# Kernel optimization log

Measured on AMD Instinct MI355X. Metric: run time of the kernel, lower is better.

Reference implementation:

```python
import jax, jax.numpy as jnp
import numpy as np

DIM = 512
NUM_HEADS = 8
HEAD_DIM = DIM // NUM_HEADS


def setup_inputs() -> dict:
    key = jax.random.key(0)
    ks = jax.random.split(key, 9)
    s = 1.0 / np.sqrt(DIM)
    x = jax.random.normal(ks[0], (2, 4096, DIM), dtype=jnp.float32)
    Wq = jax.random.uniform(ks[1], (DIM, DIM), jnp.float32, -s, s)
    bq = jax.random.uniform(ks[2], (DIM,), jnp.float32, -s, s)
    Wk = jax.random.uniform(ks[3], (DIM, DIM), jnp.float32, -s, s)
    bk = jax.random.uniform(ks[4], (DIM,), jnp.float32, -s, s)
    Wv = jax.random.uniform(ks[5], (DIM, DIM), jnp.float32, -s, s)
    bv = jax.random.uniform(ks[6], (DIM,), jnp.float32, -s, s)
    Wo = jax.random.uniform(ks[7], (DIM, DIM), jnp.float32, -s, s)
    bo = jax.random.uniform(ks[8], (DIM,), jnp.float32, -s, s)
    return {"x": x, "Wq": Wq, "bq": bq, "Wk": Wk, "bk": bk,
            "Wv": Wv, "bv": bv, "Wo": Wo, "bo": bo}


def reference(x, Wq, bq, Wk, bk, Wv, bv, Wo, bo):
    B, S, D = x.shape
    H, Hd = NUM_HEADS, HEAD_DIM
    # Linear layers (torch stores weight as [out,in]; here W is [in,out])
    q = (x @ Wq + bq).reshape(B, S, H, Hd).transpose(0, 2, 1, 3)  # [B,H,S,Hd]
    k = (x @ Wk + bk).reshape(B, S, H, Hd).transpose(0, 2, 1, 3)
    v = (x @ Wv + bv).reshape(B, S, H, Hd).transpose(0, 2, 1, 3)
    # NOTE: original scales by dim**0.5, not head_dim**0.5
    energy = jnp.einsum('bhqd,bhkd->bhqk', q, k) / jnp.sqrt(jnp.float32(D))
    attn = jax.nn.softmax(energy, axis=-1)
    out = jnp.einsum('bhqk,bhkd->bhqd', attn, v)
    out = out.transpose(0, 2, 1, 3).reshape(B, S, D)
    return out @ Wo + bo
```

## Files before the change

### kernel.cpp

```cpp
#include <hip/hip_runtime.h>

typedef unsigned short USH;
typedef short s16x8 __attribute__((ext_vector_type(8)));
typedef float f32x4 __attribute__((ext_vector_type(4)));
typedef float f32x4v __attribute__((ext_vector_type(4)));
typedef unsigned int u32x4 __attribute__((ext_vector_type(4)));
typedef s16x8 s16x8_a __attribute__((may_alias));
typedef f32x4v f32x4v_a __attribute__((may_alias));
typedef u32x4 u32x4_a __attribute__((may_alias));
typedef unsigned int u32_a __attribute__((may_alias));
typedef unsigned long long u64_a __attribute__((may_alias));

#if __has_builtin(__builtin_amdgcn_exp2f)
#define EXP2F(x) __builtin_amdgcn_exp2f(x)
#else
#define EXP2F(x) __builtin_exp2f(x)
#endif

__device__ __forceinline__ USH f2bf(float f) {
  union { float f; unsigned int i; } c; c.f = f;
  unsigned int x = c.i;
  return (USH)((x + 0x7FFFu + ((x >> 16) & 1u)) >> 16);
}
__device__ __forceinline__ unsigned int pk_bf16(float a, float b) {
  union { float f; unsigned int i; } ca, cb; ca.f = a; cb.f = b;
  return ((ca.i + 0x8000u) >> 16) | ((cb.i + 0x8000u) & 0xFFFF0000u);
}

__device__ __forceinline__ f32x4 mfma16(s16x8 a, s16x8 b, f32x4 c) {
  return __builtin_amdgcn_mfma_f32_16x16x32_bf16(a, b, c, 0, 0, 0);
}

__global__ void transpose_w(const float* __restrict__ Wq, const float* __restrict__ Wk,
                            const float* __restrict__ Wv, const float* __restrict__ Wo,
                            USH* __restrict__ wsT) {
  __shared__ float tile[32][33];
  const int z = blockIdx.z;
  const float* W = (z == 0) ? Wq : (z == 1) ? Wk : (z == 2) ? Wv : Wo;
  USH* WT = wsT + (size_t)z * 262144;
  const int n0 = blockIdx.x * 32, k0 = blockIdx.y * 32;
  const int tx = threadIdx.x, ty = threadIdx.y;
  #pragma unroll
  for (int i = 0; i < 4; ++i)
    tile[ty + i * 8][tx] = W[(size_t)(k0 + ty + i * 8) * 512 + n0 + tx];
  __syncthreads();
  #pragma unroll
  for (int i = 0; i < 4; ++i)
    WT[(size_t)(n0 + ty + i * 8) * 512 + k0 + tx] = f2bf(tile[tx][ty + i * 8]);
}

__global__ __launch_bounds__(256) void cvt_x(const float* __restrict__ x,
                                             USH* __restrict__ xb) {
  const size_t i = ((size_t)blockIdx.x * 256 + threadIdx.x) * 8;
  const f32x4v a = *(const f32x4v_a*)(x + i);
  const f32x4v b = *(const f32x4v_a*)(x + i + 4);
  u32x4 s;
  s.x = pk_bf16(a.x, a.y); s.y = pk_bf16(a.z, a.w);
  s.z = pk_bf16(b.x, b.y); s.w = pk_bf16(b.z, b.w);
  *(u32x4_a*)(xb + i) = s;
}

template <int MODE>
__global__ __launch_bounds__(256, 2) void gemm_bias(
    const USH* __restrict__ A, const USH* __restrict__ BT0,
    const float* __restrict__ b0, const float* __restrict__ b1,
    const float* __restrict__ b2,
    USH* __restrict__ oQ, USH* __restrict__ oKV, float* __restrict__ oF) {
  __shared__ __align__(16) USH As[128 * 36];
  __shared__ __align__(16) USH Bs[128 * 36];
  const int z = blockIdx.z;
  const USH* BT = BT0 + (size_t)z * 262144;
  const float* bias = (z == 0) ? b0 : ((z == 1) ? b1 : b2);
  USH* outb = (z == 0) ? oQ : (oKV + (size_t)(z - 1) * 4194304);
  const float qs = (MODE == 1 && z == 0) ? 0.06375871528132839f : 1.0f;

  const int t = threadIdx.x;
  const int w = t >> 6, lane = t & 63;
  const int c = lane & 15, g = lane >> 4;
  const int wm = w & 1, wn = w >> 1;
  const int m0 = blockIdx.x * 128, n0 = blockIdx.y * 128;
  const int srow = t >> 1, scol = (t & 1) * 16;

  f32x4 acc[4][4] = {};

  for (int kt = 0; kt < 16; ++kt) {
    __syncthreads();
    {
      const USH* Ap = A + (size_t)(m0 + srow) * 512 + kt * 32 + scol;
      const s16x8 a0 = *(const s16x8_a*)(Ap);
      const s16x8 a1 = *(const s16x8_a*)(Ap + 8);
      *(s16x8_a*)(As + srow * 36 + scol) = a0;
      *(s16x8_a*)(As + srow * 36 + scol + 8) = a1;
      const USH* Bp = BT + (size_t)(n0 + srow) * 512 + kt * 32 + scol;
      const s16x8 bb0 = *(const s16x8_a*)(Bp);
      const s16x8 bb1 = *(const s16x8_a*)(Bp + 8);
      *(s16x8_a*)(Bs + srow * 36 + scol) = bb0;
      *(s16x8_a*)(Bs + srow * 36 + scol + 8) = bb1;
    }
    __syncthreads();
    s16x8 af[4], bfr[4];
    #pragma unroll
    for (int i = 0; i < 4; ++i) {
      af[i]  = *(const s16x8_a*)(As + (wm * 64 + i * 16 + c) * 36 + g * 8);
      bfr[i] = *(const s16x8_a*)(Bs + (wn * 64 + i * 16 + c) * 36 + g * 8);
    }
    #pragma unroll
    for (int mf = 0; mf < 4; ++mf)
      #pragma unroll
      for (int nf = 0; nf < 4; ++nf)
        acc[mf][nf] = mfma16(af[mf], bfr[nf], acc[mf][nf]);
  }

  #pragma unroll
  for (int nf = 0; nf < 4; ++nf) {
    const int n = n0 + wn * 64 + nf * 16 + c;
    const float bv = bias[n];
    #pragma unroll
    for (int mf = 0; mf < 4; ++mf)
      #pragma unroll
      for (int r = 0; r < 4; ++r) {
        const int m = m0 + wm * 64 + mf * 16 + g * 4 + r;
        const float v = (acc[mf][nf][r] + bv) * qs;
        if (MODE == 0) {
          oF[(size_t)m * 512 + n] = v;
        } else {
          const int bb = m >> 12, s = m & 4095, h = n >> 6, hd = n & 63;
          outb[(((size_t)(bb * 8 + h)) * 4096 + s) * 64 + hd] = f2bf(v);
        }
      }
  }
}

__global__ __launch_bounds__(256, 2) void attn(const USH* __restrict__ Qbuf,
                                               const USH* __restrict__ kv,
                                               USH* __restrict__ att) {
  __shared__ __align__(16) USH Ks[2 * 64 * 36];
  __shared__ __align__(16) USH Vt[64 * 76];
  __shared__ __align__(16) USH Ps[4][32 * 76];
  __shared__ float lbuf[4][32];

  const int t = threadIdx.x;
  const int w = t >> 6, lane = t & 63;
  const int c = lane & 15, g = lane >> 4;
  const int bh = blockIdx.y;
  const int bb = bh >> 3, hh = bh & 7;
  const size_t base = (size_t)bh * 262144;
  const USH* Q = Qbuf + base;
  const USH* K = kv + base;
  const USH* V = kv + 4194304 + base;
  const int q0 = blockIdx.x * 128 + w * 32;

  s16x8 qf[2][2];
  #pragma unroll
  for (int colf = 0; colf < 2; ++colf)
    #pragma unroll
    for (int kh = 0; kh < 2; ++kh)
      qf[colf][kh] = *(const s16x8_a*)(Q + (size_t)(q0 + colf * 16 + c) * 64 + kh * 32 + g * 8);

  s16x8 onesf;
  {
    const short one = (short)0x3F80, val = (c == 0) ? one : (short)0;
    #pragma unroll
    for (int j = 0; j < 8; ++j) onesf[j] = val;
  }

  f32x4 o[2][4] = {};
  f32x4 o_l[2] = {};
  const int kr = t >> 2, kc = (t & 3) * 16;

  for (int kt = 0; kt < 64; ++kt) {
    __syncthreads();
    {
      const s16x8 k0 = *(const s16x8_a*)(K + (size_t)(kt * 64 + kr) * 64 + kc);
      const s16x8 k1 = *(const s16x8_a*)(K + (size_t)(kt * 64 + kr) * 64 + kc + 8);
      const int half = kc >> 5, off = kc & 31;
      *(s16x8_a*)(Ks + half * 2304 + kr * 36 + off) = k0;
      *(s16x8_a*)(Ks + half * 2304 + kr * 36 + off + 8) = k1;
    }
    {
      const int rA = 2 * (t & 31), c0v = (t >> 5) * 8;
      const s16x8 v0 = *(const s16x8_a*)(V + (size_t)(kt * 64 + rA) * 64 + c0v);
      const s16x8 v1 = *(const s16x8_a*)(V + (size_t)(kt * 64 + rA + 1) * 64 + c0v);
      #pragma unroll
      for (int j = 0; j < 8; ++j) {
        const unsigned int pk =
            (unsigned int)(USH)v0[j] | (((unsigned int)(USH)v1[j]) << 16);
        *(u32_a*)(&Vt[(c0v + j) * 76 + rA]) = pk;
      }
    }
    __syncthreads();

    f32x4 st[4][2] = {};
    #pragma unroll
    for (int kh = 0; kh < 2; ++kh) {
      s16x8 ak[4];
      #pragma unroll
      for (int kff = 0; kff < 4; ++kff)
        ak[kff] = *(const s16x8_a*)(Ks + kh * 2304 + (kff * 16 + c) * 36 + g * 8);
      #pragma unroll
      for (int kff = 0; kff < 4; ++kff)
        #pragma unroll
        for (int colf = 0; colf < 2; ++colf)
          st[kff][colf] = mfma16(ak[kff], qf[colf][kh], st[kff][colf]);
    }

    #pragma unroll
    for (int colf = 0; colf < 2; ++colf)
      #pragma unroll
      for (int kff = 0; kff < 4; ++kff)
        #pragma unroll
        for (int r = 0; r < 4; ++r)
          st[kff][colf][r] = EXP2F(st[kff][colf][r]);

    #pragma unroll
    for (int colf = 0; colf < 2; ++colf)
      #pragma unroll
      for (int kff = 0; kff < 4; ++kff) {
        const unsigned int lo = pk_bf16(st[kff][colf][0], st[kff][colf][1]);
        const unsigned int hi = pk_bf16(st[kff][colf][2], st[kff][colf][3]);
        const unsigned long long pk64 =
            (unsigned long long)lo | ((unsigned long long)hi << 32);
        *(u64_a*)(&Ps[w][(c + 16 * colf) * 76 + kff * 16 + g * 4]) = pk64;
      }

    #pragma unroll
    for (int kf = 0; kf < 2; ++kf) {
      s16x8 ap[2], bv[4];
      #pragma unroll
      for (int mf = 0; mf < 2; ++mf)
        ap[mf] = *(const s16x8_a*)(&Ps[w][(mf * 16 + c) * 76 + kf * 32 + g * 8]);
      #pragma unroll
      for (int hf = 0; hf < 4; ++hf)
        bv[hf] = *(const s16x8_a*)(&Vt[(c + 16 * hf) * 76 + kf * 32 + g * 8]);
      #pragma unroll
      for (int mf = 0; mf < 2; ++mf) {
        #pragma unroll
        for (int hf = 0; hf < 4; ++hf)
          o[mf][hf] = mfma16(ap[mf], bv[hf], o[mf][hf]);
        o_l[mf] = mfma16(ap[mf], onesf, o_l[mf]);
      }
    }
  }

  if (c == 0) {
    #pragma unroll
    for (int mf = 0; mf < 2; ++mf)
      #pragma unroll
      for (int r = 0; r < 4; ++r)
        lbuf[w][mf * 16 + g * 4 + r] = o_l[mf][r];
  }
  __syncthreads();

  #pragma unroll
  for (int mf = 0; mf < 2; ++mf)
    #pragma unroll
    for (int r = 0; r < 4; ++r) {
      const int ml = mf * 16 + g * 4 + r;
      const float linv = 1.0f / lbuf[w][ml];
      const int qrow = q0 + ml;
      #pragma unroll
      for (int hf = 0; hf < 4; ++hf) {
        const int hd = c + 16 * hf;
        att[((size_t)(bb * 4096 + qrow)) * 512 + hh * 64 + hd] =
            f2bf(o[mf][hf][r] * linv);
      }
    }
}

extern "C" void kernel_launch(void* const* d_in, const int* in_sizes, int n_in,
                              void* d_out, int out_size, void* d_ws, size_t ws_size,
                              hipStream_t stream) {
  (void)in_sizes; (void)n_in; (void)out_size; (void)ws_size;
  const float* x  = (const float*)d_in[0];
  const float* Wq = (const float*)d_in[1];
  const float* bq = (const float*)d_in[2];
  const float* Wk = (const float*)d_in[3];
  const float* bk = (const float*)d_in[4];
  const float* Wv = (const float*)d_in[5];
  const float* bv = (const float*)d_in[6];
  const float* Wo = (const float*)d_in[7];
  const float* bo = (const float*)d_in[8];
  USH* ws  = (USH*)d_ws;
  USH* wT  = ws;
  USH* kv  = ws + 1048576;
  USH* att = ws + 1048576 + 8388608;
  float* outF = (float*)d_out;
  USH* qscratch = (USH*)d_out;
  USH* xb = (USH*)d_out + 4194304;

  transpose_w<<<dim3(16, 16, 4), dim3(32, 8), 0, stream>>>(Wq, Wk, Wv, Wo, wT);
  cvt_x<<<2048, 256, 0, stream>>>(x, xb);
  gemm_bias<1><<<dim3(64, 4, 3), 256, 0, stream>>>(xb, wT, bq, bk, bv,
                                                   qscratch, kv, nullptr);
  attn<<<dim3(32, 16), 256, 0, stream>>>(qscratch, kv, att);
  gemm_bias<0><<<dim3(64, 4, 1), 256, 0, stream>>>(att, wT + 3 * 262144, bo, bo, bo,
                                                   nullptr, nullptr, outF);
}
```

Measured before the change: 232.9 us.

## Prefetch next tiles into registers and store V pre-transposed from projection

The GEMM and attention loops now load the next K-tile's global data into registers before the current tile's compute, so global latency overlaps the MFMA work. The QKV projection writes V in a transposed [bh][hd][s] layout. This lets the attention kernel copy V straight into shared memory with vector stores instead of the per-element transpose-and-pack loop. The cost is extra registers, which may lower occupancy, and strided scalar stores in the V projection epilogue.

```diff
diff --git a/kernel.cpp b/kernel.cpp
--- a/kernel.cpp
+++ b/kernel.cpp
@@ -8,7 +8,6 @@
 typedef s16x8 s16x8_a __attribute__((may_alias));
 typedef f32x4v f32x4v_a __attribute__((may_alias));
 typedef u32x4 u32x4_a __attribute__((may_alias));
-typedef unsigned int u32_a __attribute__((may_alias));
 typedef unsigned long long u64_a __attribute__((may_alias));
 
 #if __has_builtin(__builtin_amdgcn_exp2f)
@@ -83,20 +82,24 @@
 
   f32x4 acc[4][4] = {};
 
+  const USH* Ap0 = A + (size_t)(m0 + srow) * 512 + scol;
+  const USH* Bp0 = BT + (size_t)(n0 + srow) * 512 + scol;
+  s16x8 pa0 = *(const s16x8_a*)(Ap0);
+  s16x8 pa1 = *(const s16x8_a*)(Ap0 + 8);
+  s16x8 pb0 = *(const s16x8_a*)(Bp0);
+  s16x8 pb1 = *(const s16x8_a*)(Bp0 + 8);
+
   for (int kt = 0; kt < 16; ++kt) {
     __syncthreads();
-    {
-      const USH* Ap = A + (size_t)(m0 + srow) * 512 + kt * 32 + scol;
-      const s16x8 a0 = *(const s16x8_a*)(Ap);
-      const s16x8 a1 = *(const s16x8_a*)(Ap + 8);
-      *(s16x8_a*)(As + srow * 36 + scol) = a0;
-      *(s16x8_a*)(As + srow * 36 + scol + 8) = a1;
-      const USH* Bp = BT + (size_t)(n0 + srow) * 512 + kt * 32 + scol;
-      const s16x8 bb0 = *(const s16x8_a*)(Bp);
-      const s16x8 bb1 = *(const s16x8_a*)(Bp + 8);
-      *(s16x8_a*)(Bs + srow * 36 + scol) = bb0;
-      *(s16x8_a*)(Bs + srow * 36 + scol + 8) = bb1;
-    }
+    *(s16x8_a*)(As + srow * 36 + scol) = pa0;
+    *(s16x8_a*)(As + srow * 36 + scol + 8) = pa1;
+    *(s16x8_a*)(Bs + srow * 36 + scol) = pb0;
+    *(s16x8_a*)(Bs + srow * 36 + scol + 8) = pb1;
+    const int ktn = (kt < 15) ? kt + 1 : kt;
+    pa0 = *(const s16x8_a*)(Ap0 + ktn * 32);
+    pa1 = *(const s16x8_a*)(Ap0 + ktn * 32 + 8);
+    pb0 = *(const s16x8_a*)(Bp0 + ktn * 32);
+    pb1 = *(const s16x8_a*)(Bp0 + ktn * 32 + 8);
     __syncthreads();
     s16x8 af[4], bfr[4];
     #pragma unroll
@@ -125,7 +128,10 @@
           oF[(size_t)m * 512 + n] = v;
         } else {
           const int bb = m >> 12, s = m & 4095, h = n >> 6, hd = n & 63;
-          outb[(((size_t)(bb * 8 + h)) * 4096 + s) * 64 + hd] = f2bf(v);
+          if (z == 2)
+            outb[(((size_t)(bb * 8 + h)) * 64 + hd) * 4096 + s] = f2bf(v);
+          else
+            outb[(((size_t)(bb * 8 + h)) * 4096 + s) * 64 + hd] = f2bf(v);
         }
       }
   }
@@ -167,27 +173,26 @@
   f32x4 o[2][4] = {};
   f32x4 o_l[2] = {};
   const int kr = t >> 2, kc = (t & 3) * 16;
+  const USH* Kp0 = K + (size_t)kr * 64 + kc;
+  const USH* Vp0 = V + (size_t)kr * 4096 + kc;
+  const int khalf = kc >> 5, koff = kc & 31;
+
+  s16x8 pk0 = *(const s16x8_a*)(Kp0);
+  s16x8 pk1 = *(const s16x8_a*)(Kp0 + 8);
+  s16x8 pv0 = *(const s16x8_a*)(Vp0);
+  s16x8 pv1 = *(const s16x8_a*)(Vp0 + 8);
 
   for (int kt = 0; kt < 64; ++kt) {
     __syncthreads();
-    {
-      const s16x8 k0 = *(const s16x8_a*)(K + (size_t)(kt * 64 + kr) * 64 + kc);
-      const s16x8 k1 = *(const s16x8_a*)(K + (size_t)(kt * 64 + kr) * 64 + kc + 8);
-      const int half = kc >> 5, off = kc & 31;
-      *(s16x8_a*)(Ks + half * 2304 + kr * 36 + off) = k0;
-      *(s16x8_a*)(Ks + half * 2304 + kr * 36 + off + 8) = k1;
-    }
-    {
-      const int rA = 2 * (t & 31), c0v = (t >> 5) * 8;
-      const s16x8 v0 = *(const s16x8_a*)(V + (size_t)(kt * 64 + rA) * 64 + c0v);
-      const s16x8 v1 = *(const s16x8_a*)(V + (size_t)(kt * 64 + rA + 1) * 64 + c0v);
-      #pragma unroll
-      for (int j = 0; j < 8; ++j) {
-        const unsigned int pk =
-            (unsigned int)(USH)v0[j] | (((unsigned int)(USH)v1[j]) << 16);
-        *(u32_a*)(&Vt[(c0v + j) * 76 + rA]) = pk;
-      }
-    }
+    *(s16x8_a*)(Ks + khalf * 2304 + kr * 36 + koff) = pk0;
+    *(s16x8_a*)(Ks + khalf * 2304 + kr * 36 + koff + 8) = pk1;
+    *(s16x8_a*)(Vt + kr * 76 + kc) = pv0;
+    *(s16x8_a*)(Vt + kr * 76 + kc + 8) = pv1;
+    const int ktn = (kt < 63) ? kt + 1 : kt;
+    pk0 = *(const s16x8_a*)(Kp0 + (size_t)ktn * 4096);
+    pk1 = *(const s16x8_a*)(Kp0 + (size_t)ktn * 4096 + 8);
+    pv0 = *(const s16x8_a*)(Vp0 + ktn * 64);
+    pv1 = *(const s16x8_a*)(Vp0 + ktn * 64 + 8);
     __syncthreads();
 
     f32x4 st[4][2] = {};
```

Result: faster. 215.1 us (-7.7%).
